# Kernel optimization log

Measured on AMD Instinct MI355X. Metric: run time of the kernel, lower is better.

## Reference

```python
import jax, jax.numpy as jnp
import numpy as np

B, TQ, TK, D = 16, 1024, 4096, 512


def setup_inputs() -> dict:
    key = jax.random.key(0)
    k1, k2, k3 = jax.random.split(key, 3)
    decoder_output = jax.random.normal(k1, (B, TQ, D), dtype=jnp.float32)
    encoder_output = jax.random.normal(k2, (B, TK, D), dtype=jnp.float32)
    # Keras Dense(lstm_size): kernel [D, D] (glorot-ish scale), bias [D] (zeros init)
    W_a = jax.random.normal(k3, (D, D), dtype=jnp.float32) * (1.0 / np.sqrt(D))
    b_a = jnp.zeros((D,), dtype=jnp.float32)
    return {"decoder_output": decoder_output, "encoder_output": encoder_output,
            "W_a": W_a, "b_a": b_a}


def reference(decoder_output, encoder_output, W_a, b_a):
    # Luong 'general' attention:
    # proj = Dense(encoder_output)            [B, Tk, D]
    proj = jnp.einsum('bkd,de->bke', encoder_output, W_a) + b_a
    # score = dec @ proj^T                    [B, Tq, Tk]
    score = jnp.einsum('bqd,bkd->bqk', decoder_output, proj)
    # softmax over encoder time axis (tf axis=2 == last axis here)
    alignment_vector = jax.nn.softmax(score, axis=-1)
    # context = align @ encoder_output        [B, Tq, D]
    context_vector = jnp.einsum('bqk,bkd->bqd', alignment_vector, encoder_output)
    return (context_vector, alignment_vector)
```

## Files before the change

### kernel.cpp

```cpp
#include <hip/hip_runtime.h>
#include <hip/hip_bf16.h>

#define B_  16
#define TQ_ 1024
#define TK_ 4096
#define D_  512

#define BM 128
#define BN 128
#define BK 32
#define PAD 40

typedef unsigned short u16;
typedef __attribute__((ext_vector_type(8))) short short8;
typedef __attribute__((ext_vector_type(4))) float f32x4;

__device__ __forceinline__ u16 bf16_rne(float x) {
  unsigned u = __float_as_uint(x);
  u += 0x7FFFu + ((u >> 16) & 1u);
  return (u16)(u >> 16);
}
__device__ __forceinline__ float bf16_as_f32(u16 h) {
  return __uint_as_float(((unsigned)h) << 16);
}
__device__ __forceinline__ void split_f32(float x, u16& h, u16& l) {
  u16 hh = bf16_rne(x);
  h = hh;
  l = bf16_rne(x - bf16_as_f32(hh));
}

__global__ __launch_bounds__(256) void transpose_conv_kernel(
    const float* __restrict__ E, u16* __restrict__ ET)
{
  __shared__ float tile[64][65];
  const int b  = blockIdx.z;
  const int k0 = blockIdx.x * 64;
  const int d0 = blockIdx.y * 64;
  const float* Eb = E + (long long)b * TK_ * D_;
  u16* ETb = ET + (long long)b * D_ * TK_;

  const int t  = threadIdx.x;
  const int r  = t >> 2;
  const int c4 = (t & 3) * 16;

  #pragma unroll
  for (int i = 0; i < 16; i += 4) {
    float4 v = *(const float4*)&Eb[(long long)(k0 + r) * D_ + d0 + c4 + i];
    tile[r][c4 + i + 0] = v.x;
    tile[r][c4 + i + 1] = v.y;
    tile[r][c4 + i + 2] = v.z;
    tile[r][c4 + i + 3] = v.w;
  }
  __syncthreads();

  __align__(16) u16 h[16];
  #pragma unroll
  for (int i = 0; i < 16; ++i) h[i] = bf16_rne(tile[c4 + i][r]);
  uint4* dst = (uint4*)&ETb[(long long)(d0 + r) * TK_ + k0 + c4];
  dst[0] = ((const uint4*)h)[0];
  dst[1] = ((const uint4*)h)[1];
}

__global__ __launch_bounds__(256) void gemm_split_kernel(
    const float* __restrict__ A, const float* __restrict__ Bm,
    float* __restrict__ C,
    int K, int ldc,
    long long sA, long long sB, long long sC)
{
  __shared__ u16 Ah[BM * PAD];
  __shared__ u16 Al[BM * PAD];
  __shared__ u16 Bh[BN * PAD];
  __shared__ u16 Bl[BN * PAD];

  const int bz = blockIdx.z;
  const float* Ab = A  + (long long)bz * sA + (long long)(blockIdx.y * BM) * K;
  const float* Bb = Bm + (long long)bz * sB + (long long)(blockIdx.x * BN) * K;

  const int t    = threadIdx.x;
  const int r    = t >> 1;
  const int hf   = t & 1;
  const int lane = t & 63;
  const int wave = t >> 6;
  const int wr   = (wave >> 1) * 64;
  const int wc   = (wave & 1) * 64;
  const int ln   = lane & 15;
  const int qd   = lane >> 4;

  f32x4 acc[4][4];
  #pragma unroll
  for (int i = 0; i < 4; ++i)
    #pragma unroll
    for (int j = 0; j < 4; ++j) { f32x4 z = {0.f,0.f,0.f,0.f}; acc[i][j] = z; }

  const float* srcA = Ab + (long long)r * K + hf * 16;
  const float* srcB = Bb + (long long)r * K + hf * 16;
  u16* dAh = &Ah[r * PAD + hf * 16];
  u16* dAl = &Al[r * PAD + hf * 16];
  u16* dBh = &Bh[r * PAD + hf * 16];
  u16* dBl = &Bl[r * PAD + hf * 16];

  for (int k0 = 0; k0 < K; k0 += BK) {
    {
      __align__(16) u16 h[16], l[16];
      #pragma unroll
      for (int i = 0; i < 16; i += 4) {
        float4 v = *(const float4*)(srcA + k0 + i);
        split_f32(v.x, h[i+0], l[i+0]);
        split_f32(v.y, h[i+1], l[i+1]);
        split_f32(v.z, h[i+2], l[i+2]);
        split_f32(v.w, h[i+3], l[i+3]);
      }
      ((uint4*)dAh)[0] = ((const uint4*)h)[0];
      ((uint4*)dAh)[1] = ((const uint4*)h)[1];
      ((uint4*)dAl)[0] = ((const uint4*)l)[0];
      ((uint4*)dAl)[1] = ((const uint4*)l)[1];
      #pragma unroll
      for (int i = 0; i < 16; i += 4) {
        float4 v = *(const float4*)(srcB + k0 + i);
        split_f32(v.x, h[i+0], l[i+0]);
        split_f32(v.y, h[i+1], l[i+1]);
        split_f32(v.z, h[i+2], l[i+2]);
        split_f32(v.w, h[i+3], l[i+3]);
      }
      ((uint4*)dBh)[0] = ((const uint4*)h)[0];
      ((uint4*)dBh)[1] = ((const uint4*)h)[1];
      ((uint4*)dBl)[0] = ((const uint4*)l)[0];
      ((uint4*)dBl)[1] = ((const uint4*)l)[1];
    }
    __syncthreads();

    short8 fah[4], fal[4], fbh[4], fbl[4];
    #pragma unroll
    for (int i = 0; i < 4; ++i) {
      int ra = (wr + i * 16 + ln) * PAD + qd * 8;
      int rb = (wc + i * 16 + ln) * PAD + qd * 8;
      fah[i] = *(const short8*)&Ah[ra];
      fal[i] = *(const short8*)&Al[ra];
      fbh[i] = *(const short8*)&Bh[rb];
      fbl[i] = *(const short8*)&Bl[rb];
    }
    #pragma unroll
    for (int i = 0; i < 4; ++i)
      #pragma unroll
      for (int j = 0; j < 4; ++j) {
        acc[i][j] = __builtin_amdgcn_mfma_f32_16x16x32_bf16(fah[i], fbh[j], acc[i][j], 0, 0, 0);
        acc[i][j] = __builtin_amdgcn_mfma_f32_16x16x32_bf16(fah[i], fbl[j], acc[i][j], 0, 0, 0);
        acc[i][j] = __builtin_amdgcn_mfma_f32_16x16x32_bf16(fal[i], fbh[j], acc[i][j], 0, 0, 0);
      }
    __syncthreads();
  }

  float* Cb = C + (long long)bz * sC;
  const int m0 = blockIdx.y * BM;
  const int n0 = blockIdx.x * BN;
  #pragma unroll
  for (int i = 0; i < 4; ++i)
    #pragma unroll
    for (int j = 0; j < 4; ++j)
      #pragma unroll
      for (int rg = 0; rg < 4; ++rg) {
        int row = m0 + wr + i * 16 + qd * 4 + rg;
        int col = n0 + wc + j * 16 + ln;
        Cb[(long long)row * ldc + col] = acc[i][j][rg];
      }
}

__global__ __launch_bounds__(256) void softmax_kernel(float* __restrict__ P)
{
  __shared__ float red[8];
  float* p = P + (long long)blockIdx.x * TK_;
  const int t    = threadIdx.x;
  const int lane = t & 63;
  const int wave = t >> 6;

  float4 v[4];
  float mx = -3.0e38f;
  #pragma unroll
  for (int i = 0; i < 4; ++i) {
    v[i] = *(const float4*)&p[i * 1024 + t * 4];
    mx = fmaxf(mx, fmaxf(fmaxf(v[i].x, v[i].y), fmaxf(v[i].z, v[i].w)));
  }
  #pragma unroll
  for (int o = 32; o > 0; o >>= 1) mx = fmaxf(mx, __shfl_xor(mx, o, 64));
  if (lane == 0) red[wave] = mx;
  __syncthreads();
  mx = fmaxf(fmaxf(red[0], red[1]), fmaxf(red[2], red[3]));

  float s = 0.f;
  #pragma unroll
  for (int i = 0; i < 4; ++i) {
    v[i].x = __expf(v[i].x - mx);
    v[i].y = __expf(v[i].y - mx);
    v[i].z = __expf(v[i].z - mx);
    v[i].w = __expf(v[i].w - mx);
    s += (v[i].x + v[i].y) + (v[i].z + v[i].w);
  }
  #pragma unroll
  for (int o = 32; o > 0; o >>= 1) s += __shfl_xor(s, o, 64);
  if (lane == 0) red[4 + wave] = s;
  __syncthreads();
  s = (red[4] + red[5]) + (red[6] + red[7]);
  const float inv = 1.0f / s;

  #pragma unroll
  for (int i = 0; i < 4; ++i) {
    v[i].x *= inv; v[i].y *= inv; v[i].z *= inv; v[i].w *= inv;
    *(float4*)&p[i * 1024 + t * 4] = v[i];
  }
}

__global__ __launch_bounds__(256) void gemm_ctx_kernel(
    const float* __restrict__ P, const u16* __restrict__ ET,
    float* __restrict__ C)
{
  __shared__ u16 Ahs[BM * PAD];
  __shared__ u16 Bhs[BN * PAD];

  const int bz = blockIdx.z;
  const float* Pb = P  + (long long)bz * TQ_ * TK_ + (long long)(blockIdx.y * BM) * TK_;
  const u16*   Eb = ET + (long long)bz * D_ * TK_  + (long long)(blockIdx.x * BN) * TK_;

  const int t    = threadIdx.x;
  const int r    = t >> 1;
  const int hf   = t & 1;
  const int lane = t & 63;
  const int wave = t >> 6;
  const int wr   = (wave >> 1) * 64;
  const int wc   = (wave & 1) * 64;
  const int ln   = lane & 15;
  const int qd   = lane >> 4;

  f32x4 acc[4][4];
  #pragma unroll
  for (int i = 0; i < 4; ++i)
    #pragma unroll
    for (int j = 0; j < 4; ++j) { f32x4 z = {0.f,0.f,0.f,0.f}; acc[i][j] = z; }

  const float* srcA = Pb + (long long)r * TK_ + hf * 16;
  const u16*   srcB = Eb + (long long)r * TK_ + hf * 16;
  u16* dA = &Ahs[r * PAD + hf * 16];
  u16* dB = &Bhs[r * PAD + hf * 16];

  for (int k0 = 0; k0 < TK_; k0 += BK) {
    {
      __align__(16) u16 h[16];
      #pragma unroll
      for (int i = 0; i < 16; i += 4) {
        float4 v = *(const float4*)(srcA + k0 + i);
        h[i+0] = bf16_rne(v.x);
        h[i+1] = bf16_rne(v.y);
        h[i+2] = bf16_rne(v.z);
        h[i+3] = bf16_rne(v.w);
      }
      ((uint4*)dA)[0] = ((const uint4*)h)[0];
      ((uint4*)dA)[1] = ((const uint4*)h)[1];
      const uint4* sb = (const uint4*)(srcB + k0);
      ((uint4*)dB)[0] = sb[0];
      ((uint4*)dB)[1] = sb[1];
    }
    __syncthreads();

    short8 fa[4], fb[4];
    #pragma unroll
    for (int i = 0; i < 4; ++i) {
      fa[i] = *(const short8*)&Ahs[(wr + i * 16 + ln) * PAD + qd * 8];
      fb[i] = *(const short8*)&Bhs[(wc + i * 16 + ln) * PAD + qd * 8];
    }
    #pragma unroll
    for (int i = 0; i < 4; ++i)
      #pragma unroll
      for (int j = 0; j < 4; ++j)
        acc[i][j] = __builtin_amdgcn_mfma_f32_16x16x32_bf16(fa[i], fb[j], acc[i][j], 0, 0, 0);
    __syncthreads();
  }

  float* Cb = C + (long long)bz * TQ_ * D_;
  const int m0 = blockIdx.y * BM;
  const int n0 = blockIdx.x * BN;
  #pragma unroll
  for (int i = 0; i < 4; ++i)
    #pragma unroll
    for (int j = 0; j < 4; ++j)
      #pragma unroll
      for (int rg = 0; rg < 4; ++rg) {
        int row = m0 + wr + i * 16 + qd * 4 + rg;
        int col = n0 + wc + j * 16 + ln;
        Cb[(long long)row * D_ + col] = acc[i][j][rg];
      }
}

extern "C" void kernel_launch(void* const* d_in, const int* in_sizes, int n_in,
                              void* d_out, int out_size, void* d_ws, size_t ws_size,
                              hipStream_t stream) {
  (void)in_sizes; (void)n_in; (void)out_size; (void)ws_size;
  const float* dec = (const float*)d_in[0];
  const float* enc = (const float*)d_in[1];
  const float* Wa  = (const float*)d_in[2];

  float* ctx   = (float*)d_out;
  float* align = ctx + (long long)B_ * TQ_ * D_;

  float* dec2 = (float*)d_ws;
  u16*   encT = (u16*)((char*)d_ws + sizeof(float) * (size_t)B_ * TQ_ * D_);

  transpose_conv_kernel<<<dim3(TK_ / 64, D_ / 64, B_), 256, 0, stream>>>(enc, encT);

  gemm_split_kernel<<<dim3(D_ / BN, (B_ * TQ_) / BM, 1), 256, 0, stream>>>(
      dec, Wa, dec2, D_, D_, 0, 0, 0);

  gemm_split_kernel<<<dim3(TK_ / BN, TQ_ / BM, B_), 256, 0, stream>>>(
      dec2, enc, align, D_, TK_,
      (long long)TQ_ * D_, (long long)TK_ * D_, (long long)TQ_ * TK_);

  softmax_kernel<<<B_ * TQ_, 256, 0, stream>>>(align);

  gemm_ctx_kernel<<<dim3(D_ / BN, TQ_ / BM, B_), 256, 0, stream>>>(align, encT, ctx);
}
```

Measured before the change: 1.035 ms.

## Switch GEMMs to fp16 with two-term split and direct global-to-LDS loads

The score GEMM now takes the decoder projection pre-split into fp16 hi/lo halves, written by the first GEMM's epilogue. Encoder rows are rounded to a single fp16 term, so each tile issues 2 MFMAs instead of 3 bf16 split products. Operand tiles are loaded with global_load_lds, which skips register staging. The context GEMM uses fp16 with a 64x256 tile over 512 threads. This trades some accuracy in the encoder-side rounding for fewer matrix ops and less conversion work, and it also risks LDS bank conflicts because the padding was removed.

```diff
diff --git a/kernel.cpp b/kernel.cpp
--- a/kernel.cpp
+++ b/kernel.cpp
@@ -6,13 +6,9 @@
 #define TK_ 4096
 #define D_  512
 
-#define BM 128
-#define BN 128
-#define BK 32
-#define PAD 40
-
 typedef unsigned short u16;
 typedef __attribute__((ext_vector_type(8))) short short8;
+typedef __attribute__((ext_vector_type(8))) _Float16 f16x8;
 typedef __attribute__((ext_vector_type(4))) float f32x4;
 
 __device__ __forceinline__ u16 bf16_rne(float x) {
@@ -23,21 +19,27 @@
 __device__ __forceinline__ float bf16_as_f32(u16 h) {
   return __uint_as_float(((unsigned)h) << 16);
 }
-__device__ __forceinline__ void split_f32(float x, u16& h, u16& l) {
+__device__ __forceinline__ void split_bf16(float x, u16& h, u16& l) {
   u16 hh = bf16_rne(x);
   h = hh;
   l = bf16_rne(x - bf16_as_f32(hh));
 }
 
+__device__ __forceinline__ void glld16(const void* g, void* lds) {
+  __builtin_amdgcn_global_load_lds(
+      (const __attribute__((address_space(1))) unsigned int*)g,
+      (__attribute__((address_space(3))) unsigned int*)lds, 16, 0, 0);
+}
+
 __global__ __launch_bounds__(256) void transpose_conv_kernel(
-    const float* __restrict__ E, u16* __restrict__ ET)
+    const float* __restrict__ E, _Float16* __restrict__ ET)
 {
   __shared__ float tile[64][65];
   const int b  = blockIdx.z;
   const int k0 = blockIdx.x * 64;
   const int d0 = blockIdx.y * 64;
   const float* Eb = E + (long long)b * TK_ * D_;
-  u16* ETb = ET + (long long)b * D_ * TK_;
+  _Float16* ETb = ET + (long long)b * D_ * TK_;
 
   const int t  = threadIdx.x;
   const int r  = t >> 2;
@@ -53,28 +55,30 @@
   }
   __syncthreads();
 
-  __align__(16) u16 h[16];
-  #pragma unroll
-  for (int i = 0; i < 16; ++i) h[i] = bf16_rne(tile[c4 + i][r]);
+  __align__(16) _Float16 h[16];
+  #pragma unroll
+  for (int i = 0; i < 16; ++i) h[i] = (_Float16)tile[c4 + i][r];
   uint4* dst = (uint4*)&ETb[(long long)(d0 + r) * TK_ + k0 + c4];
   dst[0] = ((const uint4*)h)[0];
   dst[1] = ((const uint4*)h)[1];
 }
 
-__global__ __launch_bounds__(256) void gemm_split_kernel(
+#define DBM 128
+#define DBN 128
+#define DBK 32
+#define DPAD 40
+
+__global__ __launch_bounds__(256) void gemm_dec2_kernel(
     const float* __restrict__ A, const float* __restrict__ Bm,
-    float* __restrict__ C,
-    int K, int ldc,
-    long long sA, long long sB, long long sC)
+    _Float16* __restrict__ Ch, _Float16* __restrict__ Cl)
 {
-  __shared__ u16 Ah[BM * PAD];
-  __shared__ u16 Al[BM * PAD];
-  __shared__ u16 Bh[BN * PAD];
-  __shared__ u16 Bl[BN * PAD];
-
-  const int bz = blockIdx.z;
-  const float* Ab = A  + (long long)bz * sA + (long long)(blockIdx.y * BM) * K;
-  const float* Bb = Bm + (long long)bz * sB + (long long)(blockIdx.x * BN) * K;
+  __shared__ u16 Ah[DBM * DPAD];
+  __shared__ u16 Al[DBM * DPAD];
+  __shared__ u16 Bh[DBN * DPAD];
+  __shared__ u16 Bl[DBN * DPAD];
+
+  const float* Ab = A  + (long long)(blockIdx.y * DBM) * D_;
+  const float* Bb = Bm + (long long)(blockIdx.x * DBN) * D_;
 
   const int t    = threadIdx.x;
   const int r    = t >> 1;
@@ -92,23 +96,23 @@
     #pragma unroll
     for (int j = 0; j < 4; ++j) { f32x4 z = {0.f,0.f,0.f,0.f}; acc[i][j] = z; }
 
-  const float* srcA = Ab + (long long)r * K + hf * 16;
-  const float* srcB = Bb + (long long)r * K + hf * 16;
-  u16* dAh = &Ah[r * PAD + hf * 16];
-  u16* dAl = &Al[r * PAD + hf * 16];
-  u16* dBh = &Bh[r * PAD + hf * 16];
-  u16* dBl = &Bl[r * PAD + hf * 16];
-
-  for (int k0 = 0; k0 < K; k0 += BK) {
+  const float* srcA = Ab + (long long)r * D_ + hf * 16;
+  const float* srcB = Bb + (long long)r * D_ + hf * 16;
+  u16* dAh = &Ah[r * DPAD + hf * 16];
+  u16* dAl = &Al[r * DPAD + hf * 16];
+  u16* dBh = &Bh[r * DPAD + hf * 16];
+  u16* dBl = &Bl[r * DPAD + hf * 16];
+
+  for (int k0 = 0; k0 < D_; k0 += DBK) {
     {
       __align__(16) u16 h[16], l[16];
       #pragma unroll
       for (int i = 0; i < 16; i += 4) {
         float4 v = *(const float4*)(srcA + k0 + i);
-        split_f32(v.x, h[i+0], l[i+0]);
-        split_f32(v.y, h[i+1], l[i+1]);
-        split_f32(v.z, h[i+2], l[i+2]);
-        split_f32(v.w, h[i+3], l[i+3]);
+        split_bf16(v.x, h[i+0], l[i+0]);
+        split_bf16(v.y, h[i+1], l[i+1]);
+        split_bf16(v.z, h[i+2], l[i+2]);
+        split_bf16(v.w, h[i+3], l[i+3]);
       }
       ((uint4*)dAh)[0] = ((const uint4*)h)[0];
       ((uint4*)dAh)[1] = ((const uint4*)h)[1];
@@ -117,10 +121,10 @@
       #pragma unroll
       for (int i = 0; i < 16; i += 4) {
         float4 v = *(const float4*)(srcB + k0 + i);
-        split_f32(v.x, h[i+0], l[i+0]);
-        split_f32(v.y, h[i+1], l[i+1]);
-        split_f32(v.z, h[i+2], l[i+2]);
-        split_f32(v.w, h[i+3], l[i+3]);
+        split_bf16(v.x, h[i+0], l[i+0]);
+        split_bf16(v.y, h[i+1], l[i+1]);
+        split_bf16(v.z, h[i+2], l[i+2]);
+        split_bf16(v.w, h[i+3], l[i+3]);
       }
       ((uint4*)dBh)[0] = ((const uint4*)h)[0];
       ((uint4*)dBh)[1] = ((const uint4*)h)[1];
@@ -132,8 +136,8 @@
     short8 fah[4], fal[4], fbh[4], fbl[4];
     #pragma unroll
     for (int i = 0; i < 4; ++i) {
-      int ra = (wr + i * 16 + ln) * PAD + qd * 8;
-      int rb = (wc + i * 16 + ln) * PAD + qd * 8;
+      int ra = (wr + i * 16 + ln) * DPAD + qd * 8;
+      int rb = (wc + i * 16 + ln) * DPAD + qd * 8;
       fah[i] = *(const short8*)&Ah[ra];
       fal[i] = *(const short8*)&Al[ra];
       fbh[i] = *(const short8*)&Bh[rb];
@@ -150,9 +154,8 @@
     __syncthreads();
   }
 
-  float* Cb = C + (long long)bz * sC;
-  const int m0 = blockIdx.y * BM;
-  const int n0 = blockIdx.x * BN;
+  const int m0 = blockIdx.y * DBM;
+  const int n0 = blockIdx.x * DBN;
   #pragma unroll
   for (int i = 0; i < 4; ++i)
     #pragma unroll
@@ -161,7 +164,111 @@
       for (int rg = 0; rg < 4; ++rg) {
         int row = m0 + wr + i * 16 + qd * 4 + rg;
         int col = n0 + wc + j * 16 + ln;
-        Cb[(long long)row * ldc + col] = acc[i][j][rg];
+        float x = acc[i][j][rg];
+        _Float16 h = (_Float16)x;
+        _Float16 l = (_Float16)(x - (float)h);
+        long long idx = (long long)row * D_ + col;
+        Ch[idx] = h;
+        Cl[idx] = l;
+      }
+}
+
+#define SBM 128
+#define SBN 128
+#define SBK 32
+
+__global__ __launch_bounds__(256) void gemm_score_kernel(
+    const _Float16* __restrict__ A_h, const _Float16* __restrict__ A_l,
+    const float* __restrict__ Bf, float* __restrict__ C)
+{
+  __shared__ _Float16 sAh[SBM * SBK];
+  __shared__ _Float16 sAl[SBM * SBK];
+  __shared__ _Float16 sB [SBN * SBK];
+
+  const int bz = blockIdx.z;
+  const int m0 = blockIdx.y * SBM;
+  const int n0 = blockIdx.x * SBN;
+  const _Float16* Ahb = A_h + (long long)bz * TQ_ * D_ + (long long)m0 * D_;
+  const _Float16* Alb = A_l + (long long)bz * TQ_ * D_ + (long long)m0 * D_;
+  const float*    Bb  = Bf  + (long long)bz * TK_ * D_ + (long long)n0 * D_;
+
+  const int t    = threadIdx.x;
+  const int lane = t & 63;
+  const int wave = t >> 6;
+  const int wr   = (wave >> 1) * 64;
+  const int wc   = (wave & 1) * 64;
+  const int ln   = lane & 15;
+  const int qd   = lane >> 4;
+
+  f32x4 acc[4][4];
+  #pragma unroll
+  for (int i = 0; i < 4; ++i)
+    #pragma unroll
+    for (int j = 0; j < 4; ++j) { f32x4 z = {0.f,0.f,0.f,0.f}; acc[i][j] = z; }
+
+  const int c0   = wave * 2;
+  const int arow = c0 * 16 + (lane >> 2);
+  const int ab   = (lane & 3) * 16;
+  const char* gAh = (const char*)Ahb + (long long)arow * D_ * 2 + ab;
+  const char* gAl = (const char*)Alb + (long long)arow * D_ * 2 + ab;
+  const long long rstep = (long long)16 * D_ * 2;
+  char* lAh = (char*)sAh + c0 * 1024 + lane * 16;
+  char* lAl = (char*)sAl + c0 * 1024 + lane * 16;
+
+  const int brow = t >> 1;
+  const int bhf  = t & 1;
+  const float* srcB = Bb + (long long)brow * D_ + bhf * 16;
+  _Float16* dB = &sB[brow * SBK + bhf * 16];
+
+  for (int k0 = 0; k0 < D_; k0 += SBK) {
+    glld16(gAh + (long long)k0 * 2, lAh);
+    glld16(gAh + (long long)k0 * 2 + rstep, lAh + 1024);
+    glld16(gAl + (long long)k0 * 2, lAl);
+    glld16(gAl + (long long)k0 * 2 + rstep, lAl + 1024);
+    {
+      __align__(16) _Float16 hb[16];
+      #pragma unroll
+      for (int i = 0; i < 16; i += 4) {
+        float4 v = *(const float4*)(srcB + k0 + i);
+        hb[i+0] = (_Float16)v.x;
+        hb[i+1] = (_Float16)v.y;
+        hb[i+2] = (_Float16)v.z;
+        hb[i+3] = (_Float16)v.w;
+      }
+      ((uint4*)dB)[0] = ((const uint4*)hb)[0];
+      ((uint4*)dB)[1] = ((const uint4*)hb)[1];
+    }
+    __syncthreads();
+
+    f16x8 fah[4], fal[4], fb[4];
+    #pragma unroll
+    for (int i = 0; i < 4; ++i) {
+      int ra = (wr + i * 16 + ln) * SBK + qd * 8;
+      int rb = (wc + i * 16 + ln) * SBK + qd * 8;
+      fah[i] = *(const f16x8*)&sAh[ra];
+      fal[i] = *(const f16x8*)&sAl[ra];
+      fb[i]  = *(const f16x8*)&sB[rb];
+    }
+    #pragma unroll
+    for (int i = 0; i < 4; ++i)
+      #pragma unroll
+      for (int j = 0; j < 4; ++j) {
+        acc[i][j] = __builtin_amdgcn_mfma_f32_16x16x32_f16(fah[i], fb[j], acc[i][j], 0, 0, 0);
+        acc[i][j] = __builtin_amdgcn_mfma_f32_16x16x32_f16(fal[i], fb[j], acc[i][j], 0, 0, 0);
+      }
+    __syncthreads();
+  }
+
+  float* Cb = C + (long long)bz * TQ_ * TK_;
+  #pragma unroll
+  for (int i = 0; i < 4; ++i)
+    #pragma unroll
+    for (int j = 0; j < 4; ++j)
+      #pragma unroll
+      for (int rg = 0; rg < 4; ++rg) {
+        int row = m0 + wr + i * 16 + qd * 4 + rg;
+        int col = n0 + wc + j * 16 + ln;
+        Cb[(long long)row * TK_ + col] = acc[i][j][rg];
       }
 }
 
@@ -209,76 +316,81 @@
   }
 }
 
-__global__ __launch_bounds__(256) void gemm_ctx_kernel(
-    const float* __restrict__ P, const u16* __restrict__ ET,
+#define CBM 64
+#define CBN 256
+#define CBK 32
+
+__global__ __launch_bounds__(512) void gemm_ctx_kernel(
+    const float* __restrict__ P, const _Float16* __restrict__ ET,
     float* __restrict__ C)
 {
-  __shared__ u16 Ahs[BM * PAD];
-  __shared__ u16 Bhs[BN * PAD];
+  __shared__ _Float16 sA[CBM * CBK];
+  __shared__ _Float16 sB[CBN * CBK];
 
   const int bz = blockIdx.z;
-  const float* Pb = P  + (long long)bz * TQ_ * TK_ + (long long)(blockIdx.y * BM) * TK_;
-  const u16*   Eb = ET + (long long)bz * D_ * TK_  + (long long)(blockIdx.x * BN) * TK_;
+  const int m0 = blockIdx.y * CBM;
+  const int n0 = blockIdx.x * CBN;
+  const float*    Pb = P  + (long long)bz * TQ_ * TK_ + (long long)m0 * TK_;
+  const _Float16* Eb = ET + (long long)bz * D_ * TK_  + (long long)n0 * TK_;
 
   const int t    = threadIdx.x;
-  const int r    = t >> 1;
-  const int hf   = t & 1;
   const int lane = t & 63;
   const int wave = t >> 6;
-  const int wr   = (wave >> 1) * 64;
-  const int wc   = (wave & 1) * 64;
+  const int wr   = (wave >> 2) * 32;
+  const int wc   = (wave & 3) * 64;
   const int ln   = lane & 15;
   const int qd   = lane >> 4;
 
-  f32x4 acc[4][4];
-  #pragma unroll
-  for (int i = 0; i < 4; ++i)
+  f32x4 acc[2][4];
+  #pragma unroll
+  for (int i = 0; i < 2; ++i)
     #pragma unroll
     for (int j = 0; j < 4; ++j) { f32x4 z = {0.f,0.f,0.f,0.f}; acc[i][j] = z; }
 
-  const float* srcA = Pb + (long long)r * TK_ + hf * 16;
-  const u16*   srcB = Eb + (long long)r * TK_ + hf * 16;
-  u16* dA = &Ahs[r * PAD + hf * 16];
-  u16* dB = &Bhs[r * PAD + hf * 16];
-
-  for (int k0 = 0; k0 < TK_; k0 += BK) {
+  const int c0   = wave * 2;
+  const int brow = c0 * 16 + (lane >> 2);
+  const int bb   = (lane & 3) * 16;
+  const char* gB = (const char*)Eb + (long long)brow * TK_ * 2 + bb;
+  const long long rstep = (long long)16 * TK_ * 2;
+  char* lB = (char*)sB + c0 * 1024 + lane * 16;
+
+  const int arow = t >> 3;
+  const int aseg = t & 7;
+  const float* gA = Pb + (long long)arow * TK_ + aseg * 4;
+  _Float16* lA = &sA[arow * CBK + aseg * 4];
+
+  for (int k0 = 0; k0 < TK_; k0 += CBK) {
+    glld16(gB + (long long)k0 * 2, lB);
+    glld16(gB + (long long)k0 * 2 + rstep, lB + 1024);
     {
-      __align__(16) u16 h[16];
-      #pragma unroll
-      for (int i = 0; i < 16; i += 4) {
-        float4 v = *(const float4*)(srcA + k0 + i);
-        h[i+0] = bf16_rne(v.x);
-        h[i+1] = bf16_rne(v.y);
-        h[i+2] = bf16_rne(v.z);
-        h[i+3] = bf16_rne(v.w);
-      }
-      ((uint4*)dA)[0] = ((const uint4*)h)[0];
-      ((uint4*)dA)[1] = ((const uint4*)h)[1];
-      const uint4* sb = (const uint4*)(srcB + k0);
-      ((uint4*)dB)[0] = sb[0];
-      ((uint4*)dB)[1] = sb[1];
+      float4 v = *(const float4*)(gA + k0);
+      union { _Float16 h[4]; uint2 u; } pk;
+      pk.h[0] = (_Float16)v.x;
+      pk.h[1] = (_Float16)v.y;
+      pk.h[2] = (_Float16)v.z;
+      pk.h[3] = (_Float16)v.w;
+      *(uint2*)lA = pk.u;
     }
     __syncthreads();
 
-    short8 fa[4], fb[4];
-    #pragma unroll
-    for (int i = 0; i < 4; ++i) {
-      fa[i] = *(const short8*)&Ahs[(wr + i * 16 + ln) * PAD + qd * 8];
-      fb[i] = *(const short8*)&Bhs[(wc + i * 16 + ln) * PAD + qd * 8];
-    }
-    #pragma unroll
-    for (int i = 0; i < 4; ++i)
+    f16x8 fa[2], fb[4];
+    #pragma unroll
+    for (int i = 0; i < 2; ++i)
+      fa[i] = *(const f16x8*)&sA[(wr + i * 16 + ln) * CBK + qd * 8];
+    #pragma unroll
+    for (int j = 0; j < 4; ++j)
+      fb[j] = *(const f16x8*)&sB[(wc + j * 16 + ln) * CBK + qd * 8];
+    #pragma unroll
+    for (int i = 0; i < 2; ++i)
       #pragma unroll
       for (int j = 0; j < 4; ++j)
-        acc[i][j] = __builtin_amdgcn_mfma_f32_16x16x32_bf16(fa[i], fb[j], acc[i][j], 0, 0, 0);
+        acc[i][j] = __builtin_amdgcn_mfma_f32_16x16x32_f16(fa[i], fb[j], acc[i][j], 0, 0, 0);
     __syncthreads();
   }
 
   float* Cb = C + (long long)bz * TQ_ * D_;
-  const int m0 = blockIdx.y * BM;
-  const int n0 = blockIdx.x * BN;
-  #pragma unroll
-  for (int i = 0; i < 4; ++i)
+  #pragma unroll
+  for (int i = 0; i < 2; ++i)
     #pragma unroll
     for (int j = 0; j < 4; ++j)
       #pragma unroll
@@ -300,19 +412,19 @@
   float* ctx   = (float*)d_out;
   float* align = ctx + (long long)B_ * TQ_ * D_;
 
-  float* dec2 = (float*)d_ws;
-  u16*   encT = (u16*)((char*)d_ws + sizeof(float) * (size_t)B_ * TQ_ * D_);
+  _Float16* dec2h = (_Float16*)d_ws;
+  _Float16* dec2l = dec2h + (size_t)B_ * TQ_ * D_;
+  _Float16* encT  = dec2l + (size_t)B_ * TQ_ * D_;
 
   transpose_conv_kernel<<<dim3(TK_ / 64, D_ / 64, B_), 256, 0, stream>>>(enc, encT);
 
-  gemm_split_kernel<<<dim3(D_ / BN, (B_ * TQ_) / BM, 1), 256, 0, stream>>>(
-      dec, Wa, dec2, D_, D_, 0, 0, 0);
-
-  gemm_split_kernel<<<dim3(TK_ / BN, TQ_ / BM, B_), 256, 0, stream>>>(
-      dec2, enc, align, D_, TK_,
-      (long long)TQ_ * D_, (long long)TK_ * D_, (long long)TQ_ * TK_);
+  gemm_dec2_kernel<<<dim3(D_ / DBN, (B_ * TQ_) / DBM, 1), 256, 0, stream>>>(
+      dec, Wa, dec2h, dec2l);
+
+  gemm_score_kernel<<<dim3(TK_ / SBN, TQ_ / SBM, B_), 256, 0, stream>>>(
+      dec2h, dec2l, enc, align);
 
   softmax_kernel<<<B_ * TQ_, 256, 0, stream>>>(align);
 
-  gemm_ctx_kernel<<<dim3(D_ / BN, TQ_ / BM, B_), 256, 0, stream>>>(align, encT, ctx);
-}
+  gemm_ctx_kernel<<<dim3(D_ / CBN, TQ_ / CBM, B_), 512, 0, stream>>>(align, encT, ctx);
+}
```

After: 891.5 us. 1.16x faster.
